# Kernel tuning notes

Measured on AMD Instinct MI355X. Metric: run time of the kernel, lower is better.

Reference implementation:

```python
import jax, jax.numpy as jnp
import numpy as np

DIA = 2  # dilation of the 3x3 shift pattern


def setup_inputs() -> dict:
    key = jax.random.key(0)
    ks = jax.random.split(key, 6)
    B, C, H, W = 8, 3, 512, 512
    return {
        "x": jax.random.normal(ks[0], (B, C, H, W), dtype=jnp.float32),
        "y": jax.random.normal(ks[1], (B, C, 2 * H, 2 * W), dtype=jnp.float32),
        "w1": jax.random.normal(ks[2], (C,), dtype=jnp.float32) * 0.1,
        "b1": jax.random.normal(ks[3], (C,), dtype=jnp.float32) * 0.1,
        "w2": jax.random.normal(ks[4], (C,), dtype=jnp.float32) * 0.1,
        "b2": jax.random.normal(ks[5], (C,), dtype=jnp.float32) * 0.1,
    }


def _per_channel(x, w, b):
    # grouped 1x1 conv with groups == channels == per-channel scale + bias
    return x * w[None, :, None, None] + b[None, :, None, None]


def reference(x, y, w1, b1, w2, b2):
    D = DIA
    h, w = x.shape[2], x.shape[3]
    # conv1 is applied twice to the same input -> x_o == x_r
    x_o = jax.nn.relu(_per_channel(x, w1, b1))
    x_r = x_o
    # 9-way shifted zero-padded sum == dilated 3x3 box-sum
    pad = jnp.pad(x_o, ((0, 0), (0, 0), (D, D), (D, D)))
    out_n = jnp.zeros_like(x_o)
    for i in range(3):
        for j in range(3):
            out_n = out_n + pad[:, :, i * D:i * D + h, j * D:j * D + w]
    gate = jax.nn.sigmoid(_per_channel(out_n, w2, b2))
    out = gate * x_r
    # F.interpolate default mode='nearest': src = floor(dst * in / out)
    H2, W2 = y.shape[2], y.shape[3]
    ih = (jnp.arange(H2) * h) // H2
    iw = (jnp.arange(W2) * w) // W2
    up = out[:, :, ih, :][:, :, :, iw]
    return y + up
```

## Files before the change

kernel.cpp:

```cpp
#include <hip/hip_runtime.h>


#define DIA 2

__global__ __launch_bounds__(256) void shift_block_up_kernel(
    const float* __restrict__ x, const float* __restrict__ y,
    const float* __restrict__ w1v, const float* __restrict__ b1v,
    const float* __restrict__ w2v, const float* __restrict__ b2v,
    float* __restrict__ out)
{
    constexpr int C = 3, H = 512, W = 512;
    constexpr int W2 = 1024;

    int idx = blockIdx.x * blockDim.x + threadIdx.x;
    int wp = idx & (W / 2 - 1);
    int h  = (idx >> 8) & (H - 1);
    int bc = idx >> 17;
    int c  = bc % C;
    int w0 = wp * 2;

    const float s_w1 = w1v[c], s_b1 = b1v[c];
    const float s_w2 = w2v[c], s_b2 = b2v[c];

    const float* xp = x + (size_t)bc * (size_t)(H * W);

    float sum0 = 0.f, sum1 = 0.f;
    float xo0 = 0.f, xo1 = 0.f;

    #pragma unroll
    for (int i = 0; i < 3; ++i) {
        int hh = h + (i - 1) * DIA;
        bool hok = (unsigned)hh < (unsigned)H;
        const float* row = xp + (size_t)hh * W;
        #pragma unroll
        for (int j = 0; j < 3; ++j) {
            int wa = w0 + (j - 1) * DIA;
            int wb = wa + 1;
            float va = (hok && (unsigned)wa < (unsigned)W)
                         ? fmaxf(row[wa] * s_w1 + s_b1, 0.f) : 0.f;
            float vb = (hok && (unsigned)wb < (unsigned)W)
                         ? fmaxf(row[wb] * s_w1 + s_b1, 0.f) : 0.f;
            sum0 += va;
            sum1 += vb;
            if (i == 1 && j == 1) { xo0 = va; xo1 = vb; }
        }
    }

    float z0 = sum0 * s_w2 + s_b2;
    float z1 = sum1 * s_w2 + s_b2;
    float g0 = 1.f / (1.f + __expf(-z0));
    float g1 = 1.f / (1.f + __expf(-z1));
    float o0 = g0 * xo0;
    float o1 = g1 * xo1;

    size_t obase = (size_t)bc * (size_t)(2 * H) * W2
                 + (size_t)(2 * h) * W2 + (size_t)(2 * w0);
    float4 ya = *(const float4*)(y + obase);
    float4 yb = *(const float4*)(y + obase + W2);
    *(float4*)(out + obase)      = make_float4(ya.x + o0, ya.y + o0, ya.z + o1, ya.w + o1);
    *(float4*)(out + obase + W2) = make_float4(yb.x + o0, yb.y + o0, yb.z + o1, yb.w + o1);
}

extern "C" void kernel_launch(void* const* d_in, const int* in_sizes, int n_in,
                              void* d_out, int out_size, void* d_ws, size_t ws_size,
                              hipStream_t stream) {
    const float* x  = (const float*)d_in[0];
    const float* y  = (const float*)d_in[1];
    const float* w1 = (const float*)d_in[2];
    const float* b1 = (const float*)d_in[3];
    const float* w2 = (const float*)d_in[4];
    const float* b2 = (const float*)d_in[5];
    float* out = (float*)d_out;

    constexpr int B = 8, C = 3, H = 512, W = 512;
    int total_threads = B * C * H * (W / 2);
    int block = 256;
    int grid = total_threads / block;
    shift_block_up_kernel<<<grid, block, 0, stream>>>(x, y, w1, b1, w2, b2, out);
}
```

Before: 220.7 us.

## Process eight pixels per thread with vectorized loads and nontemporal stores

```diff
diff --git a/kernel.cpp b/kernel.cpp
--- a/kernel.cpp
+++ b/kernel.cpp
@@ -3,62 +3,119 @@
 
 #define DIA 2
 
-__global__ __launch_bounds__(256) void shift_block_up_kernel(
+typedef float floatx4 __attribute__((ext_vector_type(4)));
+
+__global__ __launch_bounds__(256) void fused_kernel(
     const float* __restrict__ x, const float* __restrict__ y,
     const float* __restrict__ w1v, const float* __restrict__ b1v,
     const float* __restrict__ w2v, const float* __restrict__ b2v,
     float* __restrict__ out)
 {
-    constexpr int C = 3, H = 512, W = 512;
-    constexpr int W2 = 1024;
+    constexpr int C = 3, H = 512, W = 512, W2 = 1024;
 
     int idx = blockIdx.x * blockDim.x + threadIdx.x;
-    int wp = idx & (W / 2 - 1);
-    int h  = (idx >> 8) & (H - 1);
-    int bc = idx >> 17;
+    int t  = idx & 63;
+    int h  = __builtin_amdgcn_readfirstlane((idx >> 6) & (H - 1));
+    int bc = __builtin_amdgcn_readfirstlane(idx >> 15);
     int c  = bc % C;
-    int w0 = wp * 2;
+    int w0 = t << 3;
 
     const float s_w1 = w1v[c], s_b1 = b1v[c];
     const float s_w2 = w2v[c], s_b2 = b2v[c];
 
-    const float* xp = x + (size_t)bc * (size_t)(H * W);
+    const float* __restrict__ xrow = x + ((size_t)bc * H + (size_t)h) * W + w0;
+    const float* r0 = xrow - DIA * W;
+    const float* r2 = xrow + DIA * W;
 
-    float sum0 = 0.f, sum1 = 0.f;
-    float xo0 = 0.f, xo1 = 0.f;
+    const bool lok = (t > 0), rok = (t < 63);
+    const bool ok0 = (h >= DIA), ok2 = (h < H - DIA);
+    const float mlf = lok ? 1.f : 0.f;
+    const float mrf = rok ? 1.f : 0.f;
+    const float m0  = ok0 ? 1.f : 0.f;
+    const float m2  = ok2 ? 1.f : 0.f;
 
+    const float2 Z2 = make_float2(0.f, 0.f);
+    const float4 Z4 = make_float4(0.f, 0.f, 0.f, 0.f);
+
+    float2 L1 = lok ? *(const float2*)(xrow - 2) : Z2;
+    float4 A1 = *(const float4*)(xrow);
+    float4 B1 = *(const float4*)(xrow + 4);
+    float2 R1 = rok ? *(const float2*)(xrow + 8) : Z2;
+
+    float2 L0 = (ok0 && lok) ? *(const float2*)(r0 - 2) : Z2;
+    float4 A0 = ok0 ? *(const float4*)(r0) : Z4;
+    float4 B0 = ok0 ? *(const float4*)(r0 + 4) : Z4;
+    float2 R0 = (ok0 && rok) ? *(const float2*)(r0 + 8) : Z2;
+
+    float2 L2 = (ok2 && lok) ? *(const float2*)(r2 - 2) : Z2;
+    float4 A2 = ok2 ? *(const float4*)(r2) : Z4;
+    float4 B2 = ok2 ? *(const float4*)(r2 + 4) : Z4;
+    float2 R2 = (ok2 && rok) ? *(const float2*)(r2 + 8) : Z2;
+
+    size_t obase = (((size_t)bc * (2 * H) + (size_t)(2 * h)) * W2) + (size_t)(w0 << 1);
+    const float* yp0 = y + obase;
+    const float* yp1 = yp0 + W2;
+    float4 y00 = *(const float4*)(yp0);
+    float4 y01 = *(const float4*)(yp0 + 4);
+    float4 y02 = *(const float4*)(yp0 + 8);
+    float4 y03 = *(const float4*)(yp0 + 12);
+    float4 y10 = *(const float4*)(yp1);
+    float4 y11 = *(const float4*)(yp1 + 4);
+    float4 y12 = *(const float4*)(yp1 + 8);
+    float4 y13 = *(const float4*)(yp1 + 12);
+
+    float vs[8] = {0.f,0.f,0.f,0.f,0.f,0.f,0.f,0.f};
+    float ctr[8];
+
+    auto row = [&](float2 L, float4 A, float4 B, float2 R,
+                   float mL, float mM, float mR, float* center) {
+        float a[12];
+        a[0]  = mL * fmaxf(fmaf(L.x, s_w1, s_b1), 0.f);
+        a[1]  = mL * fmaxf(fmaf(L.y, s_w1, s_b1), 0.f);
+        a[2]  = mM * fmaxf(fmaf(A.x, s_w1, s_b1), 0.f);
+        a[3]  = mM * fmaxf(fmaf(A.y, s_w1, s_b1), 0.f);
+        a[4]  = mM * fmaxf(fmaf(A.z, s_w1, s_b1), 0.f);
+        a[5]  = mM * fmaxf(fmaf(A.w, s_w1, s_b1), 0.f);
+        a[6]  = mM * fmaxf(fmaf(B.x, s_w1, s_b1), 0.f);
+        a[7]  = mM * fmaxf(fmaf(B.y, s_w1, s_b1), 0.f);
+        a[8]  = mM * fmaxf(fmaf(B.z, s_w1, s_b1), 0.f);
+        a[9]  = mM * fmaxf(fmaf(B.w, s_w1, s_b1), 0.f);
+        a[10] = mR * fmaxf(fmaf(R.x, s_w1, s_b1), 0.f);
+        a[11] = mR * fmaxf(fmaf(R.y, s_w1, s_b1), 0.f);
+        if (center) {
+            #pragma unroll
+            for (int p = 0; p < 8; ++p) center[p] = a[p + 2];
+        }
+        #pragma unroll
+        for (int p = 0; p < 8; ++p) vs[p] += a[p] + a[p + 2] + a[p + 4];
+    };
+
+    row(L0, A0, B0, R0, m0 * mlf, m0, m0 * mrf, nullptr);
+    row(L1, A1, B1, R1, mlf,      1.f, mrf,     ctr);
+    row(L2, A2, B2, R2, m2 * mlf, m2, m2 * mrf, nullptr);
+
+    float o[8];
     #pragma unroll
-    for (int i = 0; i < 3; ++i) {
-        int hh = h + (i - 1) * DIA;
-        bool hok = (unsigned)hh < (unsigned)H;
-        const float* row = xp + (size_t)hh * W;
-        #pragma unroll
-        for (int j = 0; j < 3; ++j) {
-            int wa = w0 + (j - 1) * DIA;
-            int wb = wa + 1;
-            float va = (hok && (unsigned)wa < (unsigned)W)
-                         ? fmaxf(row[wa] * s_w1 + s_b1, 0.f) : 0.f;
-            float vb = (hok && (unsigned)wb < (unsigned)W)
-                         ? fmaxf(row[wb] * s_w1 + s_b1, 0.f) : 0.f;
-            sum0 += va;
-            sum1 += vb;
-            if (i == 1 && j == 1) { xo0 = va; xo1 = vb; }
-        }
+    for (int p = 0; p < 8; ++p) {
+        float zv = fmaf(vs[p], s_w2, s_b2);
+        float g  = 1.f / (1.f + __expf(-zv));
+        o[p] = g * ctr[p];
     }
 
-    float z0 = sum0 * s_w2 + s_b2;
-    float z1 = sum1 * s_w2 + s_b2;
-    float g0 = 1.f / (1.f + __expf(-z0));
-    float g1 = 1.f / (1.f + __expf(-z1));
-    float o0 = g0 * xo0;
-    float o1 = g1 * xo1;
-
-    size_t obase = (size_t)bc * (size_t)(2 * H) * W2
-                 + (size_t)(2 * h) * W2 + (size_t)(2 * w0);
-    float4 ya = *(const float4*)(y + obase);
-    float4 yb = *(const float4*)(y + obase + W2);
-    *(float4*)(out + obase)      = make_float4(ya.x + o0, ya.y + o0, ya.z + o1, ya.w + o1);
-    *(float4*)(out + obase + W2) = make_float4(yb.x + o0, yb.y + o0, yb.z + o1, yb.w + o1);
+    float* op0 = out + obase;
+    float* op1 = op0 + W2;
+    auto nt4 = [](float* p, float a, float b, float c2, float d) {
+        floatx4 v = {a, b, c2, d};
+        __builtin_nontemporal_store(v, (floatx4*)p);
+    };
+    nt4(op0,      y00.x+o[0], y00.y+o[0], y00.z+o[1], y00.w+o[1]);
+    nt4(op0 + 4,  y01.x+o[2], y01.y+o[2], y01.z+o[3], y01.w+o[3]);
+    nt4(op0 + 8,  y02.x+o[4], y02.y+o[4], y02.z+o[5], y02.w+o[5]);
+    nt4(op0 + 12, y03.x+o[6], y03.y+o[6], y03.z+o[7], y03.w+o[7]);
+    nt4(op1,      y10.x+o[0], y10.y+o[0], y10.z+o[1], y10.w+o[1]);
+    nt4(op1 + 4,  y11.x+o[2], y11.y+o[2], y11.z+o[3], y11.w+o[3]);
+    nt4(op1 + 8,  y12.x+o[4], y12.y+o[4], y12.z+o[5], y12.w+o[5]);
+    nt4(op1 + 12, y13.x+o[6], y13.y+o[6], y13.z+o[7], y13.w+o[7]);
 }
 
 extern "C" void kernel_launch(void* const* d_in, const int* in_sizes, int n_in,
@@ -73,8 +130,8 @@
     float* out = (float*)d_out;
 
     constexpr int B = 8, C = 3, H = 512, W = 512;
-    int total_threads = B * C * H * (W / 2);
+    int total_threads = B * C * H * (W / 8);
     int block = 256;
-    int grid = total_threads / block;
-    shift_block_up_kernel<<<grid, block, 0, stream>>>(x, y, w1, b1, w2, b2, out);
+    int grid  = total_threads / block;
+    fused_kernel<<<grid, block, 0, stream>>>(x, y, w1, b1, w2, b2, out);
 }
```

New measurement: 303.8 us. 37.7% more time.
